# Kernel tuning notes

Measured on AMD Instinct MI355X. Metric: run time of the kernel, lower is better.

Reference implementation:

```python
import jax, jax.numpy as jnp
import numpy as np

NUM_HEAD = 8

def conv1x1(x, W, b):
    # x: (n, c, h, w); W: (o, c); b: (o,)
    return jnp.einsum('nchw,oc->nohw', x, W) + b[None, :, None, None]

def setup_inputs() -> dict:
    key = jax.random.key(0)
    ks = jax.random.split(key, 9)
    n, C, H, Wd = 16, 512, 64, 64
    KC, VC = 256, 512
    s = lambda fan_in: 1.0 / np.sqrt(fan_in)
    return {
        'x':  jax.random.normal(ks[0], (n, C, H, Wd), dtype=jnp.float32),
        'Wk': jax.random.normal(ks[1], (KC, C), dtype=jnp.float32) * s(C),
        'bk': jnp.zeros((KC,), dtype=jnp.float32),
        'Wq': jax.random.normal(ks[2], (KC, C), dtype=jnp.float32) * s(C),
        'bq': jnp.zeros((KC,), dtype=jnp.float32),
        'Wv': jax.random.normal(ks[3], (VC, C), dtype=jnp.float32) * s(C),
        'bv': jnp.zeros((VC,), dtype=jnp.float32),
        'We': jax.random.normal(ks[4], (C, VC), dtype=jnp.float32) * s(VC),
        'be': jnp.zeros((C,), dtype=jnp.float32),
    }

def reference(x, Wk, bk, Wq, bq, Wv, bv, We, be):
    n, c, h, w = x.shape
    L = h * w
    Hn = NUM_HEAD
    key   = conv1x1(x, Wk, bk).reshape(n, Hn, -1, L)   # (n, H, hk, L)
    query = conv1x1(x, Wq, bq).reshape(n, Hn, -1, L)   # (n, H, hk, L)
    value = conv1x1(x, Wv, bv).reshape(n, Hn, -1, L)   # (n, H, hv, L)
    key_sm   = jax.nn.softmax(key, axis=3)              # softmax over spatial
    query_sm = jax.nn.softmax(query, axis=2)            # softmax over head channels
    # linear attention: (value @ key^T) @ query, no LxL matrix
    context = jnp.einsum('nhvl,nhkl->nhvk', value, key_sm)     # (n, H, hv, hk)
    att = jnp.einsum('nhvk,nhkl->nhvl', context, query_sm)     # (n, H, hv, L)
    att = att.reshape(n, -1, h, w)                              # (n, VC, h, w)
    return x + conv1x1(att, We, be)
```

## Files before the change

kernel.cpp:

```cpp
#include <hip/hip_runtime.h>
#include <cstddef>
#include <cstdint>

#define N_BATCH 16
#define C_IN    512
#define L       4096
#define KC      256
#define VC      512
#define NH      8
#define HK      32
#define HV      64
#define CTX_CHUNKS 8
#define CHUNK_L (L / CTX_CHUNKS)

using f32x4 = __attribute__((ext_vector_type(4))) float;
using s16x8 = __attribute__((ext_vector_type(8))) short;

static __device__ inline ushort f2bf(float f) {
  uint32_t u = __float_as_uint(f);
  uint32_t r = (u + 0x7FFFu + ((u >> 16) & 1u)) >> 16;
  return (ushort)r;
}
static __device__ inline float bf2f(ushort u) {
  return __uint_as_float((uint32_t)u << 16);
}

__global__ __launch_bounds__(256) void k_prep_w(
    const float* __restrict__ Wk, const float* __restrict__ bk,
    const float* __restrict__ Wq, const float* __restrict__ bq,
    const float* __restrict__ Wv, const float* __restrict__ bv,
    ushort* __restrict__ Wb, float* __restrict__ bb)
{
  const int o = blockIdx.x;
  const float* src; const float* bsrc; int oo;
  if (o < 256)      { src = Wk + (size_t)o * C_IN;         bsrc = bk; oo = o; }
  else if (o < 512) { src = Wq + (size_t)(o - 256) * C_IN; bsrc = bq; oo = o - 256; }
  else              { src = Wv + (size_t)(o - 512) * C_IN; bsrc = bv; oo = o - 512; }
  const int t = threadIdx.x;
  Wb[(size_t)o * C_IN + t * 2]     = f2bf(src[t * 2]);
  Wb[(size_t)o * C_IN + t * 2 + 1] = f2bf(src[t * 2 + 1]);
  if (t == 0) bb[o] = bsrc[oo];
}

__global__ __launch_bounds__(256) void k_prep_x(const float* __restrict__ x,
                                                ushort* __restrict__ xT)
{
  __shared__ float t[64][65];
  const int n = blockIdx.z, cy = blockIdx.y, lx = blockIdx.x;
  const float* xp = x + ((size_t)n * C_IN + cy * 64) * L + (size_t)lx * 64;
  const int l4 = (threadIdx.x & 15) * 4;
  const int c0 = threadIdx.x >> 4;
  #pragma unroll
  for (int i = 0; i < 4; ++i) {
    int cc = c0 + i * 16;
    f32x4 v = *(const f32x4*)&xp[(size_t)cc * L + l4];
    t[cc][l4]     = v[0];
    t[cc][l4 + 1] = v[1];
    t[cc][l4 + 2] = v[2];
    t[cc][l4 + 3] = v[3];
  }
  __syncthreads();
  ushort* op = xT + ((size_t)n * L + lx * 64) * C_IN + cy * 64;
  const int cp = (threadIdx.x & 31) * 2, l0 = threadIdx.x >> 5;
  #pragma unroll
  for (int i = 0; i < 8; ++i) {
    int lr = l0 + i * 8;
    uint32_t pack = (uint32_t)f2bf(t[cp][lr]) | ((uint32_t)f2bf(t[cp + 1][lr]) << 16);
    *(uint32_t*)(op + (size_t)lr * C_IN + cp) = pack;
  }
}

#define QBM 256
#define QBN 256
#define QBK 64

__global__ __launch_bounds__(512) void k_qkv_mfma(
    const ushort* __restrict__ Wb,
    const ushort* __restrict__ xT,
    const float* __restrict__ bb,
    ushort* __restrict__ kqv,
    ushort* __restrict__ qT)
{
  extern __shared__ __align__(16) char smem[];
  const int n  = blockIdx.z;
  const int oy = blockIdx.y;
  const int lx = blockIdx.x;
  const int tid  = threadIdx.x;
  const int wave = tid >> 6, lane = tid & 63;
  const int wr = wave >> 2, wc = wave & 3;

  f32x4 acc[8][4] = {};

  const ushort* gA = Wb + (size_t)(oy * QBM) * C_IN;
  const ushort* gB = xT + ((size_t)n * L + lx * QBN) * C_IN;

  const int srow = lane >> 3;
  const int sslotbase = lane & 7;

  #define QSTAGE(buf, k0)                                                        \
    {                                                                            \
      ushort* As_ = (ushort*)(smem + (buf) * 65536);                             \
      ushort* Bs_ = (ushort*)(smem + (buf) * 65536 + 32768);                     \
      _Pragma("unroll")                                                          \
      for (int i_ = 0; i_ < 4; ++i_) {                                           \
        int rbase_ = wave * 32 + i_ * 8;                                         \
        int row_ = rbase_ + srow;                                                \
        int ss_ = sslotbase ^ (row_ & 7);                                        \
        __builtin_amdgcn_global_load_lds(                                        \
            (const __attribute__((address_space(1))) uint32_t*)(gA + (size_t)row_ * C_IN + (k0) + ss_ * 8), \
            (__attribute__((address_space(3))) uint32_t*)(As_ + rbase_ * QBK),   \
            16, 0, 0);                                                           \
        __builtin_amdgcn_global_load_lds(                                        \
            (const __attribute__((address_space(1))) uint32_t*)(gB + (size_t)row_ * C_IN + (k0) + ss_ * 8), \
            (__attribute__((address_space(3))) uint32_t*)(Bs_ + rbase_ * QBK),   \
            16, 0, 0);                                                           \
      }                                                                          \
    }

  QSTAGE(0, 0)
  __syncthreads();

  const int nt = C_IN / QBK;
  for (int t = 0; t < nt; ++t) {
    if (t < nt - 1) QSTAGE((t + 1) & 1, (t + 1) * QBK)
    ushort* As = (ushort*)(smem + (t & 1) * 65536);
    ushort* Bs = (ushort*)(smem + (t & 1) * 65536 + 32768);
    __builtin_amdgcn_s_setprio(1);
    #pragma unroll
    for (int ks = 0; ks < 2; ++ks) {
      s16x8 af[8], bfr[4];
      #pragma unroll
      for (int m = 0; m < 8; ++m) {
        int row = wr * 128 + m * 16 + (lane & 15);
        int slot = (ks * 4 + (lane >> 4)) ^ (row & 7);
        af[m] = *(const s16x8*)&As[row * QBK + slot * 8];
      }
      #pragma unroll
      for (int nn = 0; nn < 4; ++nn) {
        int row = wc * 64 + nn * 16 + (lane & 15);
        int slot = (ks * 4 + (lane >> 4)) ^ (row & 7);
        bfr[nn] = *(const s16x8*)&Bs[row * QBK + slot * 8];
      }
      #pragma unroll
      for (int m = 0; m < 8; ++m)
        #pragma unroll
        for (int nn = 0; nn < 4; ++nn)
          acc[m][nn] = __builtin_amdgcn_mfma_f32_16x16x32_bf16(af[m], bfr[nn], acc[m][nn], 0, 0, 0);
    }
    __builtin_amdgcn_s_setprio(0);
    __syncthreads();
  }
  #undef QSTAGE

  if (oy != 1) {
    float* ep = (float*)smem + wave * (16 * 68);
    const int erow = lane >> 4;
    const int ecol = lane & 15;
    const float* bias = bb + oy * QBM + wr * 128;
    ushort* outp = kqv + ((size_t)n * 1024 + oy * QBM + wr * 128) * L
                 + (size_t)lx * QBN + wc * 64;
    #pragma unroll
    for (int m = 0; m < 8; ++m) {
      #pragma unroll
      for (int nn = 0; nn < 4; ++nn)
        #pragma unroll
        for (int r = 0; r < 4; ++r)
          ep[(erow * 4 + r) * 68 + nn * 16 + ecol] = acc[m][nn][r];
      #pragma unroll
      for (int p = 0; p < 4; ++p) {
        int row = p * 4 + erow;
        f32x4 v = *(const f32x4*)&ep[row * 68 + ecol * 4];
        float bo = bias[m * 16 + row];
        uint2 pk;
        pk.x = (uint32_t)f2bf(v[0] + bo) | ((uint32_t)f2bf(v[1] + bo) << 16);
        pk.y = (uint32_t)f2bf(v[2] + bo) | ((uint32_t)f2bf(v[3] + bo) << 16);
        *(uint2*)&outp[(size_t)(m * 16 + row) * L + ecol * 4] = pk;
      }
    }
  } else {
    const float* bias = bb + 256 + wr * 128;
    ushort* qbase = qT + (size_t)n * L * KC;
    const int g4 = (lane >> 4) * 4;
    #pragma unroll
    for (int hp = 0; hp < 4; ++hp) {
      const int m0 = 2 * hp, m1 = 2 * hp + 1;
      const float b0_0 = bias[m0 * 16 + g4 + 0], b0_1 = bias[m0 * 16 + g4 + 1];
      const float b0_2 = bias[m0 * 16 + g4 + 2], b0_3 = bias[m0 * 16 + g4 + 3];
      const float b1_0 = bias[m1 * 16 + g4 + 0], b1_1 = bias[m1 * 16 + g4 + 1];
      const float b1_2 = bias[m1 * 16 + g4 + 2], b1_3 = bias[m1 * 16 + g4 + 3];
      #pragma unroll
      for (int nn = 0; nn < 4; ++nn) {
        float v0[4], v1[4];
        v0[0] = acc[m0][nn][0] + b0_0; v0[1] = acc[m0][nn][1] + b0_1;
        v0[2] = acc[m0][nn][2] + b0_2; v0[3] = acc[m0][nn][3] + b0_3;
        v1[0] = acc[m1][nn][0] + b1_0; v1[1] = acc[m1][nn][1] + b1_1;
        v1[2] = acc[m1][nn][2] + b1_2; v1[3] = acc[m1][nn][3] + b1_3;
        float mx = fmaxf(fmaxf(fmaxf(v0[0], v0[1]), fmaxf(v0[2], v0[3])),
                         fmaxf(fmaxf(v1[0], v1[1]), fmaxf(v1[2], v1[3])));
        mx = fmaxf(mx, __shfl_xor(mx, 16));
        mx = fmaxf(mx, __shfl_xor(mx, 32));
        float e0[4], e1[4];
        float s = 0.f;
        #pragma unroll
        for (int r = 0; r < 4; ++r) { e0[r] = __expf(v0[r] - mx); s += e0[r]; }
        #pragma unroll
        for (int r = 0; r < 4; ++r) { e1[r] = __expf(v1[r] - mx); s += e1[r]; }
        s += __shfl_xor(s, 16);
        s += __shfl_xor(s, 32);
        float inv = 1.0f / s;
        int l = lx * QBN + wc * 64 + nn * 16 + (lane & 15);
        ushort* dst = qbase + (size_t)l * KC + wr * 128;
        uint2 p0, p1;
        p0.x = (uint32_t)f2bf(e0[0] * inv) | ((uint32_t)f2bf(e0[1] * inv) << 16);
        p0.y = (uint32_t)f2bf(e0[2] * inv) | ((uint32_t)f2bf(e0[3] * inv) << 16);
        p1.x = (uint32_t)f2bf(e1[0] * inv) | ((uint32_t)f2bf(e1[1] * inv) << 16);
        p1.y = (uint32_t)f2bf(e1[2] * inv) | ((uint32_t)f2bf(e1[3] * inv) << 16);
        *(uint2*)&dst[m0 * 16 + g4] = p0;
        *(uint2*)&dst[m1 * 16 + g4] = p1;
      }
    }
  }
}

__device__ inline float blockReduceMax(float v, float* red) {
  #pragma unroll
  for (int off = 32; off > 0; off >>= 1)
    v = fmaxf(v, __shfl_down(v, off, 64));
  int tid = threadIdx.x;
  if ((tid & 63) == 0) red[tid >> 6] = v;
  __syncthreads();
  return fmaxf(fmaxf(red[0], red[1]), fmaxf(red[2], red[3]));
}
__device__ inline float blockReduceSum(float v, float* red) {
  #pragma unroll
  for (int off = 32; off > 0; off >>= 1)
    v += __shfl_down(v, off, 64);
  int tid = threadIdx.x;
  if ((tid & 63) == 0) red[tid >> 6] = v;
  __syncthreads();
  return red[0] + red[1] + red[2] + red[3];
}

__global__ __launch_bounds__(256) void k_kstats(const ushort* __restrict__ kqv,
                                                float* __restrict__ kmax,
                                                float* __restrict__ kinv)
{
  const int r = blockIdx.x;
  const int n = blockIdx.y;
  const ushort* row = kqv + ((size_t)n * 1024 + r) * L;
  __shared__ float red1[4];
  __shared__ float red2[4];
  const int tid = threadIdx.x;
  s16x8 a = *(const s16x8*)(row + tid * 16);
  s16x8 b = *(const s16x8*)(row + tid * 16 + 8);
  float v[16];
  #pragma unroll
  for (int j = 0; j < 8; ++j) { v[j] = bf2f((ushort)a[j]); v[8 + j] = bf2f((ushort)b[j]); }
  float m = -3.0e38f;
  #pragma unroll
  for (int j = 0; j < 16; ++j) m = fmaxf(m, v[j]);
  m = blockReduceMax(m, red1);
  float s = 0.f;
  #pragma unroll
  for (int j = 0; j < 16; ++j) s += __expf(v[j] - m);
  s = blockReduceSum(s, red2);
  if (tid == 0) { kmax[n * KC + r] = m; kinv[n * KC + r] = 1.0f / s; }
}

__global__ __launch_bounds__(256) void k_ctx_mfma(const ushort* __restrict__ kqv,
                                                  const float* __restrict__ kmax,
                                                  const float* __restrict__ kinv,
                                                  float* __restrict__ ctxpart)
{
  const int chunk = blockIdx.x;
  const int nh    = blockIdx.y;
  const int n = nh >> 3, h = nh & 7;
  const int tid = threadIdx.x, wave = tid >> 6, lane = tid & 63;

  __shared__ __align__(16) ushort Ks[32 * 64];
  __shared__ __align__(16) ushort Vs[64 * 64];
  __shared__ float km[32], kv[32];

  if (tid < 32) { km[tid] = kmax[nh * 32 + tid]; kv[tid] = kinv[nh * 32 + tid]; }
  __syncthreads();

  const ushort* Kp = kqv + ((size_t)n * 1024 + h * HK) * L + (size_t)chunk * CHUNK_L;
  const ushort* Vp = kqv + ((size_t)n * 1024 + 512 + h * HV) * L + (size_t)chunk * CHUNK_L;

  const int krow = tid >> 3;
  const int kslot = (tid & 7) ^ (krow & 7);
  f32x4 acc[2] = {};

  for (int step = 0; step < 8; ++step) {
    const int l0 = step * 64;
    #pragma unroll
    for (int j = 0; j < 2; ++j) {
      int vr = (j * 4 + wave) * 8 + (lane >> 3);
      int vslot = (lane & 7) ^ (vr & 7);
      __builtin_amdgcn_global_load_lds(
          (const __attribute__((address_space(1))) uint32_t*)(Vp + (size_t)vr * L + l0 + vslot * 8),
          (__attribute__((address_space(3))) uint32_t*)(Vs + (size_t)(j * 4 + wave) * 512),
          16, 0, 0);
    }
    s16x8 kvec = *(const s16x8*)(Kp + (size_t)krow * L + l0 + (tid & 7) * 8);
    float mk = km[krow], ik = kv[krow];
    s16x8 w;
    #pragma unroll
    for (int j = 0; j < 8; ++j) {
      float f = bf2f((ushort)kvec[j]);
      w[j] = (short)f2bf(__expf(f - mk) * ik);
    }
    *(s16x8*)&Ks[krow * 64 + kslot * 8] = w;
    __syncthreads();

    #pragma unroll
    for (int ks = 0; ks < 2; ++ks) {
      int arow = wave * 16 + (lane & 15);
      int aslot = (ks * 4 + (lane >> 4)) ^ (arow & 7);
      s16x8 af = *(const s16x8*)&Vs[arow * 64 + aslot * 8];
      #pragma unroll
      for (int nf = 0; nf < 2; ++nf) {
        int brow = nf * 16 + (lane & 15);
        int bslot = (ks * 4 + (lane >> 4)) ^ (brow & 7);
        s16x8 bfr = *(const s16x8*)&Ks[brow * 64 + bslot * 8];
        acc[nf] = __builtin_amdgcn_mfma_f32_16x16x32_bf16(af, bfr, acc[nf], 0, 0, 0);
      }
    }
    __syncthreads();
  }

  float* outp = ctxpart + ((size_t)nh * CTX_CHUNKS + chunk) * (HV * HK);
  #pragma unroll
  for (int nf = 0; nf < 2; ++nf) {
    #pragma unroll
    for (int r = 0; r < 4; ++r) {
      int v = wave * 16 + (lane >> 4) * 4 + r;
      int k = nf * 16 + (lane & 15);
      outp[v * HK + k] = acc[nf][r];
    }
  }
}

__global__ __launch_bounds__(256) void k_m(const float* __restrict__ ctxpart,
                                           const float* __restrict__ We,
                                           ushort* __restrict__ Mbuf)
{
  const int h = blockIdx.x;
  const int n = blockIdx.y;
  const int nh = n * 8 + h;
  const int tid = threadIdx.x;
  __shared__ float ctx[64][32];

  #pragma unroll
  for (int i = 0; i < 8; ++i) {
    int e = tid + i * 256;
    float s = 0.f;
    for (int c = 0; c < CTX_CHUNKS; ++c)
      s += ctxpart[((size_t)nh * CTX_CHUNKS + c) * (HV * HK) + e];
    ((float*)ctx)[e] = s;
  }
  __syncthreads();

  const int k  = tid & 31;
  const int og = tid >> 5;
  for (int j = 0; j < 64; ++j) {
    int o = og * 64 + j;
    const float* we = We + (size_t)o * VC + h * HV;
    float s = 0.f;
    #pragma unroll
    for (int v = 0; v < 64; ++v) s += we[v] * ctx[v][k];
    Mbuf[((size_t)n * 512 + o) * KC + h * HK + k] = f2bf(s);
  }
}

#define BM 128
#define BN 128
#define BK 32

__global__ __launch_bounds__(256) void k_final_mfma(
    const ushort* __restrict__ Mb,
    const ushort* __restrict__ qT,
    const float* __restrict__ x,
    const float* __restrict__ be,
    float* __restrict__ out)
{
  const int n  = blockIdx.z;
  const int oy = blockIdx.y;
  const int lx = blockIdx.x;
  const int tid  = threadIdx.x;
  const int wave = tid >> 6, lane = tid & 63;
  const int wr = wave >> 1, wc = wave & 1;

  __shared__ __align__(16) char smem[32768 + 17408];

  f32x4 acc[4][4] = {};

  const ushort* gA = Mb + ((size_t)n * 512 + oy * BM) * KC;
  const ushort* gB = qT + ((size_t)n * L + lx * BN) * KC;

  const int r0 = wave * 32;
  const int lrow = lane >> 2;

  #define FSTAGE(buf, k0)                                                        \
    {                                                                            \
      ushort* As_ = (ushort*)(smem + (buf) * 16384);                             \
      ushort* Bs_ = (ushort*)(smem + (buf) * 16384 + 8192);                      \
      _Pragma("unroll")                                                          \
      for (int i_ = 0; i_ < 2; ++i_) {                                           \
        int row_ = r0 + i_ * 16 + lrow;                                          \
        int ss_ = (lane & 3) ^ ((row_ >> 1) & 3);                                \
        __builtin_amdgcn_global_load_lds(                                        \
            (const __attribute__((address_space(1))) uint32_t*)(gA + (size_t)row_ * KC + (k0) + ss_ * 8), \
            (__attribute__((address_space(3))) uint32_t*)(As_ + (r0 + i_ * 16) * BK), \
            16, 0, 0);                                                           \
        __builtin_amdgcn_global_load_lds(                                        \
            (const __attribute__((address_space(1))) uint32_t*)(gB + (size_t)row_ * KC + (k0) + ss_ * 8), \
            (__attribute__((address_space(3))) uint32_t*)(Bs_ + (r0 + i_ * 16) * BK), \
            16, 0, 0);                                                           \
      }                                                                          \
    }

  FSTAGE(0, 0)
  __syncthreads();

  const int nt = KC / BK;
  for (int t = 0; t < nt; ++t) {
    if (t < nt - 1) FSTAGE((t + 1) & 1, (t + 1) * BK)
    ushort* As = (ushort*)(smem + (t & 1) * 16384);
    ushort* Bs = (ushort*)(smem + (t & 1) * 16384 + 8192);
    s16x8 af[4], bfr[4];
    #pragma unroll
    for (int m = 0; m < 4; ++m) {
      int row = wr * 64 + m * 16 + (lane & 15);
      int slot = (lane >> 4) ^ ((row >> 1) & 3);
      af[m] = *(const s16x8*)&As[row * BK + slot * 8];
    }
    #pragma unroll
    for (int nn = 0; nn < 4; ++nn) {
      int row = wc * 64 + nn * 16 + (lane & 15);
      int slot = (lane >> 4) ^ ((row >> 1) & 3);
      bfr[nn] = *(const s16x8*)&Bs[row * BK + slot * 8];
    }
    __builtin_amdgcn_s_setprio(1);
    #pragma unroll
    for (int m = 0; m < 4; ++m)
      #pragma unroll
      for (int nn = 0; nn < 4; ++nn)
        acc[m][nn] = __builtin_amdgcn_mfma_f32_16x16x32_bf16(af[m], bfr[nn], acc[m][nn], 0, 0, 0);
    __builtin_amdgcn_s_setprio(0);
    __syncthreads();
  }
  #undef FSTAGE

  float* ep = (float*)(smem + 32768) + wave * (16 * 68);
  const int erow = lane >> 4;
  const int ecol = lane & 15;
  const float* bias = be + oy * BM + wr * 64;
  const float* xp = x + ((size_t)n * 512 + oy * BM + wr * 64) * L
                  + (size_t)lx * BN + wc * 64;
  float* op = out + ((size_t)n * 512 + oy * BM + wr * 64) * L
            + (size_t)lx * BN + wc * 64;
  #pragma unroll
  for (int m = 0; m < 4; ++m) {
    #pragma unroll
    for (int nn = 0; nn < 4; ++nn)
      #pragma unroll
      for (int r = 0; r < 4; ++r)
        ep[(erow * 4 + r) * 68 + nn * 16 + ecol] = acc[m][nn][r];
    #pragma unroll
    for (int p = 0; p < 4; ++p) {
      int row = p * 4 + erow;
      f32x4 v = *(const f32x4*)&ep[row * 68 + ecol * 4];
      float bo = bias[m * 16 + row];
      f32x4 xv = *(const f32x4*)&xp[(size_t)(m * 16 + row) * L + ecol * 4];
      v = v + xv + bo;
      *(f32x4*)&op[(size_t)(m * 16 + row) * L + ecol * 4] = v;
    }
  }
}

extern "C" void kernel_launch(void* const* d_in, const int* in_sizes, int n_in,
                              void* d_out, int out_size, void* d_ws, size_t ws_size,
                              hipStream_t stream)
{
  const float* x  = (const float*)d_in[0];
  const float* Wk = (const float*)d_in[1];
  const float* bk = (const float*)d_in[2];
  const float* Wq = (const float*)d_in[3];
  const float* bq = (const float*)d_in[4];
  const float* Wv = (const float*)d_in[5];
  const float* bv = (const float*)d_in[6];
  const float* We = (const float*)d_in[7];
  const float* be = (const float*)d_in[8];
  float* out = (float*)d_out;

  char* ws = (char*)d_ws;
  size_t off = 0;
  ushort* kqv  = (ushort*)(ws + off); off += (size_t)N_BATCH * 1024 * L * 2;
  ushort* xT   = (ushort*)(ws + off); off += (size_t)N_BATCH * L * C_IN * 2;
  ushort* Wb   = (ushort*)(ws + off); off += (size_t)1024 * C_IN * 2;
  float*  bb   = (float*)(ws + off);  off += (size_t)1024 * 4;
  float*  kmax = (float*)(ws + off);  off += (size_t)N_BATCH * KC * 4;
  float*  kinv = (float*)(ws + off);  off += (size_t)N_BATCH * KC * 4;
  ushort* qT   = (ushort*)(ws + off); off += (size_t)N_BATCH * L * KC * 2;
  float*  ctxp = (float*)(ws + off);  off += (size_t)N_BATCH * NH * CTX_CHUNKS * HV * HK * 4;
  ushort* Mbuf = (ushort*)(ws + off); off += (size_t)N_BATCH * 512 * KC * 2;

  static bool attr_done = false;
  if (!attr_done) {
    (void)hipFuncSetAttribute((const void*)k_qkv_mfma,
                              hipFuncAttributeMaxDynamicSharedMemorySize, 131072);
    attr_done = true;
  }

  k_prep_w<<<dim3(1024), 256, 0, stream>>>(Wk, bk, Wq, bq, Wv, bv, Wb, bb);
  k_prep_x<<<dim3(64, 8, N_BATCH), 256, 0, stream>>>(x, xT);
  k_qkv_mfma<<<dim3(16, 4, N_BATCH), 512, 131072, stream>>>(Wb, xT, bb, kqv, qT);
  k_kstats<<<dim3(KC, N_BATCH), 256, 0, stream>>>(kqv, kmax, kinv);
  k_ctx_mfma<<<dim3(CTX_CHUNKS, N_BATCH * NH), 256, 0, stream>>>(kqv, kmax, kinv, ctxp);
  k_m<<<dim3(NH, N_BATCH), 256, 0, stream>>>(ctxp, We, Mbuf);
  k_final_mfma<<<dim3(32, 4, N_BATCH), 256, 0, stream>>>(Mbuf, qT, x, be, out);
}
```

Baseline: 262.3 us.

## Eliminate value projection by reassociating context through key-softmax times input

Stops materializing the value projection. It computes G = softmax(K) · x^T per batch with an MFMA GEMM and then folds Wv and bv into the small context computation (ctx = Wv·G^T + bv). This removes the 512-channel V GEMM over all spatial positions and its bf16 write and read. The cost is an extra bf16 copy of x, a materialized normalized-K buffer, and a heavier k_m2 scalar reduction over 512 input channels. The transposed x writes are also widened to 8-byte stores.

Result: slower. 309.5 us (+18.0%).

```diff
diff --git a/kernel.cpp b/kernel.cpp
--- a/kernel.cpp
+++ b/kernel.cpp
@@ -10,8 +10,6 @@
 #define NH      8
 #define HK      32
 #define HV      64
-#define CTX_CHUNKS 8
-#define CHUNK_L (L / CTX_CHUNKS)
 
 using f32x4 = __attribute__((ext_vector_type(4))) float;
 using s16x8 = __attribute__((ext_vector_type(8))) short;
@@ -28,14 +26,12 @@
 __global__ __launch_bounds__(256) void k_prep_w(
     const float* __restrict__ Wk, const float* __restrict__ bk,
     const float* __restrict__ Wq, const float* __restrict__ bq,
-    const float* __restrict__ Wv, const float* __restrict__ bv,
     ushort* __restrict__ Wb, float* __restrict__ bb)
 {
   const int o = blockIdx.x;
   const float* src; const float* bsrc; int oo;
-  if (o < 256)      { src = Wk + (size_t)o * C_IN;         bsrc = bk; oo = o; }
-  else if (o < 512) { src = Wq + (size_t)(o - 256) * C_IN; bsrc = bq; oo = o - 256; }
-  else              { src = Wv + (size_t)(o - 512) * C_IN; bsrc = bv; oo = o - 512; }
+  if (o < 256) { src = Wk + (size_t)o * C_IN;         bsrc = bk; oo = o; }
+  else         { src = Wq + (size_t)(o - 256) * C_IN; bsrc = bq; oo = o - 256; }
   const int t = threadIdx.x;
   Wb[(size_t)o * C_IN + t * 2]     = f2bf(src[t * 2]);
   Wb[(size_t)o * C_IN + t * 2 + 1] = f2bf(src[t * 2 + 1]);
@@ -43,11 +39,13 @@
 }
 
 __global__ __launch_bounds__(256) void k_prep_x(const float* __restrict__ x,
-                                                ushort* __restrict__ xT)
+                                                ushort* __restrict__ xT,
+                                                ushort* __restrict__ xb)
 {
   __shared__ float t[64][65];
   const int n = blockIdx.z, cy = blockIdx.y, lx = blockIdx.x;
   const float* xp = x + ((size_t)n * C_IN + cy * 64) * L + (size_t)lx * 64;
+  ushort* xbp = xb + ((size_t)n * C_IN + cy * 64) * L + (size_t)lx * 64;
   const int l4 = (threadIdx.x & 15) * 4;
   const int c0 = threadIdx.x >> 4;
   #pragma unroll
@@ -58,15 +56,22 @@
     t[cc][l4 + 1] = v[1];
     t[cc][l4 + 2] = v[2];
     t[cc][l4 + 3] = v[3];
+    uint2 pk;
+    pk.x = (uint32_t)f2bf(v[0]) | ((uint32_t)f2bf(v[1]) << 16);
+    pk.y = (uint32_t)f2bf(v[2]) | ((uint32_t)f2bf(v[3]) << 16);
+    *(uint2*)(xbp + (size_t)cc * L + l4) = pk;
   }
   __syncthreads();
   ushort* op = xT + ((size_t)n * L + lx * 64) * C_IN + cy * 64;
-  const int cp = (threadIdx.x & 31) * 2, l0 = threadIdx.x >> 5;
-  #pragma unroll
-  for (int i = 0; i < 8; ++i) {
-    int lr = l0 + i * 8;
-    uint32_t pack = (uint32_t)f2bf(t[cp][lr]) | ((uint32_t)f2bf(t[cp + 1][lr]) << 16);
-    *(uint32_t*)(op + (size_t)lr * C_IN + cp) = pack;
+  const int cp = (threadIdx.x & 15) * 4;
+  const int l0 = threadIdx.x >> 4;
+  #pragma unroll
+  for (int i = 0; i < 4; ++i) {
+    int lr = l0 + i * 16;
+    uint2 pk;
+    pk.x = (uint32_t)f2bf(t[cp][lr])     | ((uint32_t)f2bf(t[cp + 1][lr]) << 16);
+    pk.y = (uint32_t)f2bf(t[cp + 2][lr]) | ((uint32_t)f2bf(t[cp + 3][lr]) << 16);
+    *(uint2*)(op + (size_t)lr * C_IN + cp) = pk;
   }
 }
 
@@ -74,11 +79,11 @@
 #define QBN 256
 #define QBK 64
 
-__global__ __launch_bounds__(512) void k_qkv_mfma(
+__global__ __launch_bounds__(512) void k_kq_mfma(
     const ushort* __restrict__ Wb,
     const ushort* __restrict__ xT,
     const float* __restrict__ bb,
-    ushort* __restrict__ kqv,
+    ushort* __restrict__ Kbuf,
     ushort* __restrict__ qT)
 {
   extern __shared__ __align__(16) char smem[];
@@ -152,12 +157,12 @@
   }
   #undef QSTAGE
 
-  if (oy != 1) {
+  if (oy == 0) {
     float* ep = (float*)smem + wave * (16 * 68);
     const int erow = lane >> 4;
     const int ecol = lane & 15;
-    const float* bias = bb + oy * QBM + wr * 128;
-    ushort* outp = kqv + ((size_t)n * 1024 + oy * QBM + wr * 128) * L
+    const float* bias = bb + wr * 128;
+    ushort* outp = Kbuf + ((size_t)n * 256 + wr * 128) * L
                  + (size_t)lx * QBN + wc * 64;
     #pragma unroll
     for (int m = 0; m < 8; ++m) {
@@ -241,13 +246,13 @@
   return red[0] + red[1] + red[2] + red[3];
 }
 
-__global__ __launch_bounds__(256) void k_kstats(const ushort* __restrict__ kqv,
-                                                float* __restrict__ kmax,
-                                                float* __restrict__ kinv)
+__global__ __launch_bounds__(256) void k_kstats2(const ushort* __restrict__ Kbuf,
+                                                 ushort* __restrict__ Ksm)
 {
   const int r = blockIdx.x;
   const int n = blockIdx.y;
-  const ushort* row = kqv + ((size_t)n * 1024 + r) * L;
+  const ushort* row = Kbuf + ((size_t)n * 256 + r) * L;
+  ushort* orow = Ksm + ((size_t)n * 256 + r) * L;
   __shared__ float red1[4];
   __shared__ float red2[4];
   const int tid = threadIdx.x;
@@ -264,102 +269,158 @@
   #pragma unroll
   for (int j = 0; j < 16; ++j) s += __expf(v[j] - m);
   s = blockReduceSum(s, red2);
-  if (tid == 0) { kmax[n * KC + r] = m; kinv[n * KC + r] = 1.0f / s; }
-}
-
-__global__ __launch_bounds__(256) void k_ctx_mfma(const ushort* __restrict__ kqv,
-                                                  const float* __restrict__ kmax,
-                                                  const float* __restrict__ kinv,
-                                                  float* __restrict__ ctxpart)
-{
-  const int chunk = blockIdx.x;
-  const int nh    = blockIdx.y;
-  const int n = nh >> 3, h = nh & 7;
-  const int tid = threadIdx.x, wave = tid >> 6, lane = tid & 63;
-
-  __shared__ __align__(16) ushort Ks[32 * 64];
-  __shared__ __align__(16) ushort Vs[64 * 64];
-  __shared__ float km[32], kv[32];
-
-  if (tid < 32) { km[tid] = kmax[nh * 32 + tid]; kv[tid] = kinv[nh * 32 + tid]; }
+  float inv = 1.0f / s;
+  s16x8 w0, w1;
+  #pragma unroll
+  for (int j = 0; j < 8; ++j) {
+    w0[j] = (short)f2bf(__expf(v[j] - m) * inv);
+    w1[j] = (short)f2bf(__expf(v[8 + j] - m) * inv);
+  }
+  *(s16x8*)(orow + tid * 16)     = w0;
+  *(s16x8*)(orow + tid * 16 + 8) = w1;
+}
+
+#define GBK 32
+
+__global__ __launch_bounds__(256) void k_G(
+    const ushort* __restrict__ Ksm,
+    const ushort* __restrict__ xb,
+    float* __restrict__ Gp)
+{
+  const int n  = blockIdx.z;
+  const int cx = blockIdx.x;
+  const int ky = blockIdx.y >> 1;
+  const int lc = blockIdx.y & 1;
+  const int tid  = threadIdx.x;
+  const int wave = tid >> 6, lane = tid & 63;
+  const int wr = wave >> 1, wc = wave & 1;
+
+  __shared__ __align__(16) char smem[32768 + 17408];
+
+  f32x4 acc[4][4] = {};
+
+  const ushort* gA = Ksm + ((size_t)n * 256 + ky * 128) * L + lc * 2048;
+  const ushort* gB = xb  + ((size_t)n * 512 + cx * 128) * L + lc * 2048;
+
+  const int r0 = wave * 32;
+  const int lrow = lane >> 2;
+
+  #define GSTAGE(buf, k0)                                                        \
+    {                                                                            \
+      ushort* As_ = (ushort*)(smem + (buf) * 16384);                             \
+      ushort* Bs_ = (ushort*)(smem + (buf) * 16384 + 8192);                      \
+      _Pragma("unroll")                                                          \
+      for (int i_ = 0; i_ < 2; ++i_) {                                           \
+        int row_ = r0 + i_ * 16 + lrow;                                          \
+        int ss_ = (lane & 3) ^ ((row_ >> 1) & 3);                                \
+        __builtin_amdgcn_global_load_lds(                                        \
+            (const __attribute__((address_space(1))) uint32_t*)(gA + (size_t)row_ * L + (k0) + ss_ * 8), \
+            (__attribute__((address_space(3))) uint32_t*)(As_ + (r0 + i_ * 16) * GBK), \
+            16, 0, 0);                                                           \
+        __builtin_amdgcn_global_load_lds(                                        \
+            (const __attribute__((address_space(1))) uint32_t*)(gB + (size_t)row_ * L + (k0) + ss_ * 8), \
+            (__attribute__((address_space(3))) uint32_t*)(Bs_ + (r0 + i_ * 16) * GBK), \
+            16, 0, 0);                                                           \
+      }                                                                          \
+    }
+
+  GSTAGE(0, 0)
   __syncthreads();
 
-  const ushort* Kp = kqv + ((size_t)n * 1024 + h * HK) * L + (size_t)chunk * CHUNK_L;
-  const ushort* Vp = kqv + ((size_t)n * 1024 + 512 + h * HV) * L + (size_t)chunk * CHUNK_L;
-
-  const int krow = tid >> 3;
-  const int kslot = (tid & 7) ^ (krow & 7);
-  f32x4 acc[2] = {};
-
-  for (int step = 0; step < 8; ++step) {
-    const int l0 = step * 64;
-    #pragma unroll
-    for (int j = 0; j < 2; ++j) {
-      int vr = (j * 4 + wave) * 8 + (lane >> 3);
-      int vslot = (lane & 7) ^ (vr & 7);
-      __builtin_amdgcn_global_load_lds(
-          (const __attribute__((address_space(1))) uint32_t*)(Vp + (size_t)vr * L + l0 + vslot * 8),
-          (__attribute__((address_space(3))) uint32_t*)(Vs + (size_t)(j * 4 + wave) * 512),
-          16, 0, 0);
-    }
-    s16x8 kvec = *(const s16x8*)(Kp + (size_t)krow * L + l0 + (tid & 7) * 8);
-    float mk = km[krow], ik = kv[krow];
-    s16x8 w;
-    #pragma unroll
-    for (int j = 0; j < 8; ++j) {
-      float f = bf2f((ushort)kvec[j]);
-      w[j] = (short)f2bf(__expf(f - mk) * ik);
-    }
-    *(s16x8*)&Ks[krow * 64 + kslot * 8] = w;
+  const int nt = 2048 / GBK;
+  for (int t = 0; t < nt; ++t) {
+    if (t < nt - 1) GSTAGE((t + 1) & 1, (t + 1) * GBK)
+    ushort* As = (ushort*)(smem + (t & 1) * 16384);
+    ushort* Bs = (ushort*)(smem + (t & 1) * 16384 + 8192);
+    s16x8 af[4], bfr[4];
+    #pragma unroll
+    for (int m = 0; m < 4; ++m) {
+      int row = wr * 64 + m * 16 + (lane & 15);
+      int slot = (lane >> 4) ^ ((row >> 1) & 3);
+      af[m] = *(const s16x8*)&As[row * GBK + slot * 8];
+    }
+    #pragma unroll
+    for (int nn = 0; nn < 4; ++nn) {
+      int row = wc * 64 + nn * 16 + (lane & 15);
+      int slot = (lane >> 4) ^ ((row >> 1) & 3);
+      bfr[nn] = *(const s16x8*)&Bs[row * GBK + slot * 8];
+    }
+    __builtin_amdgcn_s_setprio(1);
+    #pragma unroll
+    for (int m = 0; m < 4; ++m)
+      #pragma unroll
+      for (int nn = 0; nn < 4; ++nn)
+        acc[m][nn] = __builtin_amdgcn_mfma_f32_16x16x32_bf16(af[m], bfr[nn], acc[m][nn], 0, 0, 0);
+    __builtin_amdgcn_s_setprio(0);
     __syncthreads();
-
-    #pragma unroll
-    for (int ks = 0; ks < 2; ++ks) {
-      int arow = wave * 16 + (lane & 15);
-      int aslot = (ks * 4 + (lane >> 4)) ^ (arow & 7);
-      s16x8 af = *(const s16x8*)&Vs[arow * 64 + aslot * 8];
-      #pragma unroll
-      for (int nf = 0; nf < 2; ++nf) {
-        int brow = nf * 16 + (lane & 15);
-        int bslot = (ks * 4 + (lane >> 4)) ^ (brow & 7);
-        s16x8 bfr = *(const s16x8*)&Ks[brow * 64 + bslot * 8];
-        acc[nf] = __builtin_amdgcn_mfma_f32_16x16x32_bf16(af, bfr, acc[nf], 0, 0, 0);
-      }
-    }
-    __syncthreads();
-  }
-
-  float* outp = ctxpart + ((size_t)nh * CTX_CHUNKS + chunk) * (HV * HK);
-  #pragma unroll
-  for (int nf = 0; nf < 2; ++nf) {
-    #pragma unroll
-    for (int r = 0; r < 4; ++r) {
-      int v = wave * 16 + (lane >> 4) * 4 + r;
-      int k = nf * 16 + (lane & 15);
-      outp[v * HK + k] = acc[nf][r];
-    }
-  }
-}
-
-__global__ __launch_bounds__(256) void k_m(const float* __restrict__ ctxpart,
-                                           const float* __restrict__ We,
-                                           ushort* __restrict__ Mbuf)
+  }
+  #undef GSTAGE
+
+  float* ep = (float*)(smem + 32768) + wave * (16 * 68);
+  const int erow = lane >> 4;
+  const int ecol = lane & 15;
+  float* op = Gp + (((size_t)n * 2 + lc) * 256 + ky * 128 + wr * 64) * 512
+            + cx * 128 + wc * 64;
+  #pragma unroll
+  for (int m = 0; m < 4; ++m) {
+    #pragma unroll
+    for (int nn = 0; nn < 4; ++nn)
+      #pragma unroll
+      for (int r = 0; r < 4; ++r)
+        ep[(erow * 4 + r) * 68 + nn * 16 + ecol] = acc[m][nn][r];
+    #pragma unroll
+    for (int p = 0; p < 4; ++p) {
+      int row = p * 4 + erow;
+      f32x4 v = *(const f32x4*)&ep[row * 68 + ecol * 4];
+      *(f32x4*)&op[(size_t)(m * 16 + row) * 512 + ecol * 4] = v;
+    }
+  }
+}
+
+__global__ __launch_bounds__(256) void k_m2(const float* __restrict__ Gp,
+                                            const float* __restrict__ Wv,
+                                            const float* __restrict__ bv,
+                                            const float* __restrict__ We,
+                                            ushort* __restrict__ Mbuf)
 {
   const int h = blockIdx.x;
   const int n = blockIdx.y;
-  const int nh = n * 8 + h;
   const int tid = threadIdx.x;
+  __shared__ float Gs[16][516];
   __shared__ float ctx[64][32];
 
-  #pragma unroll
-  for (int i = 0; i < 8; ++i) {
-    int e = tid + i * 256;
-    float s = 0.f;
-    for (int c = 0; c < CTX_CHUNKS; ++c)
-      s += ctxpart[((size_t)nh * CTX_CHUNKS + c) * (HV * HK) + e];
-    ((float*)ctx)[e] = s;
-  }
-  __syncthreads();
+  const float* g0 = Gp + ((size_t)n * 2 + 0) * 256 * 512 + (size_t)(h * HK) * 512;
+  const float* g1 = Gp + ((size_t)n * 2 + 1) * 256 * 512 + (size_t)(h * HK) * 512;
+
+  const int v  = tid >> 2;
+  const int kg = tid & 3;
+  const float* wvrow = Wv + (size_t)(h * HV + v) * C_IN;
+
+  #pragma unroll
+  for (int half = 0; half < 2; ++half) {
+    #pragma unroll
+    for (int i = 0; i < 32; ++i) {
+      int e = tid + i * 256;
+      int kr = e >> 9, c = e & 511;
+      int gk = half * 16 + kr;
+      Gs[kr][c] = g0[(size_t)gk * 512 + c] + g1[(size_t)gk * 512 + c];
+    }
+    __syncthreads();
+    float a0 = 0.f, a1 = 0.f, a2 = 0.f, a3 = 0.f;
+    for (int c = 0; c < C_IN; ++c) {
+      float w = wvrow[c];
+      a0 += w * Gs[kg * 4 + 0][c];
+      a1 += w * Gs[kg * 4 + 1][c];
+      a2 += w * Gs[kg * 4 + 2][c];
+      a3 += w * Gs[kg * 4 + 3][c];
+    }
+    float bvv = bv[h * HV + v];
+    ctx[v][half * 16 + kg * 4 + 0] = a0 + bvv;
+    ctx[v][half * 16 + kg * 4 + 1] = a1 + bvv;
+    ctx[v][half * 16 + kg * 4 + 2] = a2 + bvv;
+    ctx[v][half * 16 + kg * 4 + 3] = a3 + bvv;
+    __syncthreads();
+  }
 
   const int k  = tid & 31;
   const int og = tid >> 5;
@@ -368,7 +429,7 @@
     const float* we = We + (size_t)o * VC + h * HV;
     float s = 0.f;
     #pragma unroll
-    for (int v = 0; v < 64; ++v) s += we[v] * ctx[v][k];
+    for (int vv = 0; vv < 64; ++vv) s += we[vv] * ctx[vv][k];
     Mbuf[((size_t)n * 512 + o) * KC + h * HK + k] = f2bf(s);
   }
 }
@@ -496,28 +557,24 @@
 
   char* ws = (char*)d_ws;
   size_t off = 0;
-  ushort* kqv  = (ushort*)(ws + off); off += (size_t)N_BATCH * 1024 * L * 2;
+  ushort* Kbuf = (ushort*)(ws + off); off += (size_t)N_BATCH * 256 * L * 2;
+  ushort* Ksm  = (ushort*)(ws + off); off += (size_t)N_BATCH * 256 * L * 2;
   ushort* xT   = (ushort*)(ws + off); off += (size_t)N_BATCH * L * C_IN * 2;
-  ushort* Wb   = (ushort*)(ws + off); off += (size_t)1024 * C_IN * 2;
-  float*  bb   = (float*)(ws + off);  off += (size_t)1024 * 4;
-  float*  kmax = (float*)(ws + off);  off += (size_t)N_BATCH * KC * 4;
-  float*  kinv = (float*)(ws + off);  off += (size_t)N_BATCH * KC * 4;
+  ushort* xb   = (ushort*)(ws + off); off += (size_t)N_BATCH * C_IN * L * 2;
+  ushort* Wb   = (ushort*)(ws + off); off += (size_t)512 * C_IN * 2;
+  float*  bb   = (float*)(ws + off);  off += (size_t)512 * 4;
   ushort* qT   = (ushort*)(ws + off); off += (size_t)N_BATCH * L * KC * 2;
-  float*  ctxp = (float*)(ws + off);  off += (size_t)N_BATCH * NH * CTX_CHUNKS * HV * HK * 4;
+  float*  Gp   = (float*)(ws + off);  off += (size_t)N_BATCH * 2 * 256 * 512 * 4;
   ushort* Mbuf = (ushort*)(ws + off); off += (size_t)N_BATCH * 512 * KC * 2;
 
-  static bool attr_done = false;
-  if (!attr_done) {
-    (void)hipFuncSetAttribute((const void*)k_qkv_mfma,
-                              hipFuncAttributeMaxDynamicSharedMemorySize, 131072);
-    attr_done = true;
-  }
-
-  k_prep_w<<<dim3(1024), 256, 0, stream>>>(Wk, bk, Wq, bq, Wv, bv, Wb, bb);
-  k_prep_x<<<dim3(64, 8, N_BATCH), 256, 0, stream>>>(x, xT);
-  k_qkv_mfma<<<dim3(16, 4, N_BATCH), 512, 131072, stream>>>(Wb, xT, bb, kqv, qT);
-  k_kstats<<<dim3(KC, N_BATCH), 256, 0, stream>>>(kqv, kmax, kinv);
-  k_ctx_mfma<<<dim3(CTX_CHUNKS, N_BATCH * NH), 256, 0, stream>>>(kqv, kmax, kinv, ctxp);
-  k_m<<<dim3(NH, N_BATCH), 256, 0, stream>>>(ctxp, We, Mbuf);
+  (void)hipFuncSetAttribute((const void*)k_kq_mfma,
+                            hipFuncAttributeMaxDynamicSharedMemorySize, 131072);
+
+  k_prep_w<<<dim3(512), 256, 0, stream>>>(Wk, bk, Wq, bq, Wb, bb);
+  k_prep_x<<<dim3(64, 8, N_BATCH), 256, 0, stream>>>(x, xT, xb);
+  k_kq_mfma<<<dim3(16, 2, N_BATCH), 512, 131072, stream>>>(Wb, xT, bb, Kbuf, qT);
+  k_kstats2<<<dim3(KC, N_BATCH), 256, 0, stream>>>(Kbuf, Ksm);
+  k_G<<<dim3(4, 4, N_BATCH), 256, 0, stream>>>(Ksm, xb, Gp);
+  k_m2<<<dim3(NH, N_BATCH), 256, 0, stream>>>(Gp, Wv, bv, We, Mbuf);
   k_final_mfma<<<dim3(32, 4, N_BATCH), 256, 0, stream>>>(Mbuf, qT, x, be, out);
 }
```
